# Optimization experiments

Measured on AMD Instinct MI355X. Metric: run time of the kernel, lower is better.

## Reference

```python
import jax, jax.numpy as jnp
import numpy as np


def setup_inputs() -> dict:
    key = jax.random.key(0)
    ks = jax.random.split(key, 6)
    B, C, H, W = 8, 64, 256, 256  # C*C == 4096 required by conv_du
    x = jax.random.normal(ks[0], (B, C, H, W), dtype=jnp.float32)
    W1 = jax.random.normal(ks[1], (16, 4096), dtype=jnp.float32) * 0.02  # Conv2d(4096,16,1) weight
    b1 = jax.random.normal(ks[2], (16,), dtype=jnp.float32) * 0.02
    W2 = jax.random.normal(ks[3], (4096, 16), dtype=jnp.float32) * 0.02  # Conv2d(16,4096,1) weight
    b2 = jax.random.normal(ks[4], (4096,), dtype=jnp.float32) * 0.02
    gamma = jax.random.normal(ks[5], (1,), dtype=jnp.float32) * 0.1  # nn.Parameter (init zeros in torch)
    return {"x": x, "W1": W1, "b1": b1, "W2": W2, "b2": b2, "gamma": gamma}


def reference(x, W1, b1, W2, b2, gamma):
    B, C, H, W = x.shape
    xf = x.reshape(B, C, H * W)  # (B, C, N)
    # Gram matrix over channels: energy[b,c,d] = <x_c, x_d>
    energy = jnp.einsum('bcn,bdn->bcd', xf, xf)
    # Diagonal cosine normalization (diag entries are sums of squares, >= 0)
    diag = jnp.sqrt(jnp.diagonal(energy, axis1=1, axis2=2))  # (B, C)
    energy = energy / diag[:, :, None] / diag[:, None, :]
    # SE-style 1x1 conv bottleneck on flattened C*C = 4096 channels
    h = jax.nn.relu(jnp.einsum('bk,ok->bo', energy.reshape(B, C * C), W1) + b1)
    energy = (jnp.einsum('bk,ok->bo', h, W2) + b2).reshape(B, C, C)
    # max-minus trick then softmax over last dim
    energy_new = jnp.max(energy, axis=-1, keepdims=True) - energy
    attention = jax.nn.softmax(energy_new, axis=-1)  # (B, C, C)
    out = jnp.einsum('bcd,bdn->bcn', attention, xf).reshape(B, C, H, W)
    return gamma * out + x
```

## Files before the change

kernel.cpp:

```cpp
#include <hip/hip_runtime.h>
#include <hip/hip_bf16.h>

#define CCH 64
#define NPIX 65536
#define NSPLIT 128
#define NB (NPIX / NSPLIT)

typedef short bf16x8 __attribute__((ext_vector_type(8)));
typedef float f32x16 __attribute__((ext_vector_type(16)));

static __device__ inline short f2bf(float f) {
    union { __hip_bfloat16 h; short s; } u;
    u.h = __float2bfloat16(f);
    return u.s;
}

static __device__ inline bf16x8 cvt8(float4 a, float4 b) {
    bf16x8 r;
    r[0] = f2bf(a.x); r[1] = f2bf(a.y); r[2] = f2bf(a.z); r[3] = f2bf(a.w);
    r[4] = f2bf(b.x); r[5] = f2bf(b.y); r[6] = f2bf(b.z); r[7] = f2bf(b.w);
    return r;
}

__global__ __launch_bounds__(256) void gram_kernel(const float* __restrict__ x,
                                                   float* __restrict__ gram) {
    const int b    = blockIdx.y;
    const int t    = threadIdx.x;
    const int wave = t >> 6, lane = t & 63;
    const int qi = wave >> 1, qj = wave & 1;
    const int lrow = lane & 31, khalf = lane >> 5;

    const float* xb = x + (size_t)b * CCH * NPIX;
    const int n0 = blockIdx.x * NB;
    const float* pa = xb + (size_t)(32 * qi + lrow) * NPIX + n0 + khalf * 8;
    const float* pb = xb + (size_t)(32 * qj + lrow) * NPIX + n0 + khalf * 8;

    f32x16 acc = {};
    #pragma unroll 4
    for (int k = 0; k < NB; k += 16) {
        float4 a0 = *(const float4*)(pa + k);
        float4 a1 = *(const float4*)(pa + k + 4);
        float4 b0 = *(const float4*)(pb + k);
        float4 b1 = *(const float4*)(pb + k + 4);
        acc = __builtin_amdgcn_mfma_f32_32x32x16_bf16(cvt8(a0, a1), cvt8(b0, b1), acc, 0, 0, 0);
    }

    float* g = gram + b * 4096;
    #pragma unroll
    for (int r = 0; r < 16; ++r) {
        int row = 32 * qi + 4 * khalf + (r & 3) + 8 * (r >> 2);
        atomicAdd(&g[row * 64 + 32 * qj + lrow], acc[r]);
    }
}

__global__ __launch_bounds__(256) void se_softmax_kernel(const float* __restrict__ gram,
                                                         const float* __restrict__ W1,
                                                         const float* __restrict__ b1,
                                                         const float* __restrict__ W2,
                                                         const float* __restrict__ b2,
                                                         float* __restrict__ attn) {
    __shared__ float e[4096];
    __shared__ float rs[64];
    __shared__ float hbuf[16];
    __shared__ float pw[4][16];
    __shared__ float rowred[64];
    const int b = blockIdx.x;
    const int t = threadIdx.x;
    const int wave = t >> 6, lane = t & 63;
    const float* g = gram + b * 4096;

    if (t < 64) rs[t] = rsqrtf(g[t * 65]);
    __syncthreads();

    #pragma unroll
    for (int j = 0; j < 4; ++j) {
        int l = j * 1024 + 4 * t;
        float4 gv = *(const float4*)(g + l);
        int c = l >> 6, d = l & 63;
        float rc = rs[c];
        float4 ev;
        ev.x = gv.x * rc * rs[d + 0];
        ev.y = gv.y * rc * rs[d + 1];
        ev.z = gv.z * rc * rs[d + 2];
        ev.w = gv.w * rc * rs[d + 3];
        *(float4*)(e + l) = ev;
    }
    __syncthreads();

    float acc[16] = {};
    #pragma unroll
    for (int j = 0; j < 4; ++j) {
        float4 ev = *(const float4*)(e + j * 1024 + 4 * t);
        #pragma unroll
        for (int o = 0; o < 16; ++o) {
            float4 wv = *(const float4*)(W1 + o * 4096 + j * 1024 + 4 * t);
            acc[o] += wv.x * ev.x + wv.y * ev.y + wv.z * ev.z + wv.w * ev.w;
        }
    }
    #pragma unroll
    for (int o = 0; o < 16; ++o) {
        #pragma unroll
        for (int off = 1; off < 64; off <<= 1)
            acc[o] += __shfl_xor(acc[o], off);
    }
    if (lane == 0) {
        #pragma unroll
        for (int o = 0; o < 16; ++o) pw[wave][o] = acc[o];
    }
    __syncthreads();
    if (t < 16) {
        float s = b1[t] + pw[0][t] + pw[1][t] + pw[2][t] + pw[3][t];
        hbuf[t] = fmaxf(s, 0.f);
    }
    __syncthreads();

    float hv[16];
    #pragma unroll
    for (int o = 0; o < 16; ++o) hv[o] = hbuf[o];
    for (int l = t; l < 4096; l += 256) {
        const float* w = W2 + (size_t)l * 16;
        float4 w0 = *(const float4*)(w);
        float4 w1v = *(const float4*)(w + 4);
        float4 w2v = *(const float4*)(w + 8);
        float4 w3v = *(const float4*)(w + 12);
        float s = b2[l]
            + w0.x * hv[0]  + w0.y * hv[1]  + w0.z * hv[2]  + w0.w * hv[3]
            + w1v.x * hv[4] + w1v.y * hv[5] + w1v.z * hv[6] + w1v.w * hv[7]
            + w2v.x * hv[8] + w2v.y * hv[9] + w2v.z * hv[10] + w2v.w * hv[11]
            + w3v.x * hv[12] + w3v.y * hv[13] + w3v.z * hv[14] + w3v.w * hv[15];
        e[l] = s;
    }
    __syncthreads();

    {
        int r = t >> 2, q = t & 3;
        float mn = INFINITY;
        #pragma unroll
        for (int j = 0; j < 16; ++j) mn = fminf(mn, e[r * 64 + q * 16 + j]);
        mn = fminf(mn, __shfl_xor(mn, 1));
        mn = fminf(mn, __shfl_xor(mn, 2));
        if (q == 0) rowred[r] = mn;
    }
    __syncthreads();
    for (int l = t; l < 4096; l += 256) {
        int c = l >> 6;
        e[l] = expf(rowred[c] - e[l]);
    }
    __syncthreads();
    {
        int r = t >> 2, q = t & 3;
        float s = 0.f;
        #pragma unroll
        for (int j = 0; j < 16; ++j) s += e[r * 64 + q * 16 + j];
        s += __shfl_xor(s, 1);
        s += __shfl_xor(s, 2);
        if (q == 0) rowred[r] = 1.0f / s;
    }
    __syncthreads();
    float* ab = attn + b * 4096;
    for (int l = t; l < 4096; l += 256) {
        int c = l >> 6;
        ab[l] = e[l] * rowred[c];
    }
}

__global__ __launch_bounds__(256) void apply_kernel(const float* __restrict__ x,
                                                    const float* __restrict__ attn,
                                                    const float* __restrict__ gamma,
                                                    float* __restrict__ out) {
    const int b    = blockIdx.y;
    const int t    = threadIdx.x;
    const int wave = t >> 6, lane = t & 63;
    const int ci = wave >> 1, nj = wave & 1;
    const int lrow = lane & 31, khalf = lane >> 5;
    const float gm = gamma[0];
    const float* xb = x + (size_t)b * CCH * NPIX;
    float* ob = out + (size_t)b * CCH * NPIX;

    const float* arow = attn + b * 4096 + (32 * ci + lrow) * 64 + khalf * 8;
    bf16x8 afrag[4];
    #pragma unroll
    for (int ks = 0; ks < 4; ++ks) {
        float4 a0 = *(const float4*)(arow + ks * 16);
        float4 a1 = *(const float4*)(arow + ks * 16 + 4);
        afrag[ks] = cvt8(a0, a1);
    }

    const int n0 = blockIdx.x * NB;
    for (int it = 0; it < NB / 64; ++it) {
        const int nc = n0 + it * 64 + nj * 32 + lrow;
        f32x16 acc = {};
        #pragma unroll
        for (int ks = 0; ks < 4; ++ks) {
            const int r0 = ks * 16 + khalf * 8;
            bf16x8 bfrag;
            #pragma unroll
            for (int i = 0; i < 8; ++i)
                bfrag[i] = f2bf(xb[(size_t)(r0 + i) * NPIX + nc]);
            acc = __builtin_amdgcn_mfma_f32_32x32x16_bf16(afrag[ks], bfrag, acc, 0, 0, 0);
        }
        #pragma unroll
        for (int r = 0; r < 16; ++r) {
            int c = 32 * ci + 4 * khalf + (r & 3) + 8 * (r >> 2);
            size_t off = (size_t)c * NPIX + nc;
            ob[off] = gm * acc[r] + xb[off];
        }
    }
}

extern "C" void kernel_launch(void* const* d_in, const int* in_sizes, int n_in,
                              void* d_out, int out_size, void* d_ws, size_t ws_size,
                              hipStream_t stream) {
    const float* x     = (const float*)d_in[0];
    const float* W1    = (const float*)d_in[1];
    const float* b1    = (const float*)d_in[2];
    const float* W2    = (const float*)d_in[3];
    const float* b2    = (const float*)d_in[4];
    const float* gamma = (const float*)d_in[5];
    float* out = (float*)d_out;

    float* gram = (float*)d_ws;
    float* attn = gram + 8 * 4096;

    hipMemsetAsync(d_ws, 0, 8 * 4096 * sizeof(float), stream);

    gram_kernel<<<dim3(NSPLIT, 8), 256, 0, stream>>>(x, gram);
    se_softmax_kernel<<<8, 256, 0, stream>>>(gram, W1, b1, W2, b2, attn);
    apply_kernel<<<dim3(NSPLIT, 8), 256, 0, stream>>>(x, attn, gamma, out);
}
```

Measured before the change: 306.0 us.

## Stage gram tiles in shared memory and retune apply kernel grid

The gram kernel now loads each 64x64 pixel tile of x once into padded LDS with coalesced float4 loads and feeds the MFMAs from there. Previously each wave fetched its own A and B rows straight from global memory, so every element was read several times with strided per-lane access. The apply kernel gets twice as many blocks along the pixel axis, and both kernels gain occupancy hints in their launch bounds. The cost is two block barriers per tile and some LDS usage.

After: 409.0 us. 33.7% more time.

```diff
diff --git a/kernel.cpp b/kernel.cpp
--- a/kernel.cpp
+++ b/kernel.cpp
@@ -3,8 +3,11 @@
 
 #define CCH 64
 #define NPIX 65536
-#define NSPLIT 128
-#define NB (NPIX / NSPLIT)
+#define NSPLIT_G 128
+#define NB_G (NPIX / NSPLIT_G)
+#define NSPLIT_A 256
+#define NB_A (NPIX / NSPLIT_A)
+#define NPAD 68
 
 typedef short bf16x8 __attribute__((ext_vector_type(8)));
 typedef float f32x16 __attribute__((ext_vector_type(16)));
@@ -22,8 +25,9 @@
     return r;
 }
 
-__global__ __launch_bounds__(256) void gram_kernel(const float* __restrict__ x,
-                                                   float* __restrict__ gram) {
+__global__ __launch_bounds__(256, 4) void gram_kernel(const float* __restrict__ x,
+                                                      float* __restrict__ gram) {
+    __shared__ float xs[64][NPAD];
     const int b    = blockIdx.y;
     const int t    = threadIdx.x;
     const int wave = t >> 6, lane = t & 63;
@@ -31,18 +35,30 @@
     const int lrow = lane & 31, khalf = lane >> 5;
 
     const float* xb = x + (size_t)b * CCH * NPIX;
-    const int n0 = blockIdx.x * NB;
-    const float* pa = xb + (size_t)(32 * qi + lrow) * NPIX + n0 + khalf * 8;
-    const float* pb = xb + (size_t)(32 * qj + lrow) * NPIX + n0 + khalf * 8;
+    const int n0 = blockIdx.x * NB_G;
+    const int sc = t >> 4, sq = 4 * (t & 15);
 
     f32x16 acc = {};
-    #pragma unroll 4
-    for (int k = 0; k < NB; k += 16) {
-        float4 a0 = *(const float4*)(pa + k);
-        float4 a1 = *(const float4*)(pa + k + 4);
-        float4 b0 = *(const float4*)(pb + k);
-        float4 b1 = *(const float4*)(pb + k + 4);
-        acc = __builtin_amdgcn_mfma_f32_32x32x16_bf16(cvt8(a0, a1), cvt8(b0, b1), acc, 0, 0, 0);
+    for (int tile = 0; tile < NB_G / 64; ++tile) {
+        const int nt = n0 + tile * 64;
+        float4 v[4];
+        #pragma unroll
+        for (int i = 0; i < 4; ++i)
+            v[i] = *(const float4*)(xb + (size_t)(sc + 16 * i) * NPIX + nt + sq);
+        __syncthreads();
+        #pragma unroll
+        for (int i = 0; i < 4; ++i)
+            *(float4*)(&xs[sc + 16 * i][sq]) = v[i];
+        __syncthreads();
+
+        #pragma unroll
+        for (int kk = 0; kk < 64; kk += 16) {
+            const float* pa = &xs[32 * qi + lrow][kk + 8 * khalf];
+            const float* pb = &xs[32 * qj + lrow][kk + 8 * khalf];
+            float4 a0 = *(const float4*)(pa), a1 = *(const float4*)(pa + 4);
+            float4 b0 = *(const float4*)(pb), b1 = *(const float4*)(pb + 4);
+            acc = __builtin_amdgcn_mfma_f32_32x32x16_bf16(cvt8(a0, a1), cvt8(b0, b1), acc, 0, 0, 0);
+        }
     }
 
     float* g = gram + b * 4096;
@@ -164,10 +180,10 @@
     }
 }
 
-__global__ __launch_bounds__(256) void apply_kernel(const float* __restrict__ x,
-                                                    const float* __restrict__ attn,
-                                                    const float* __restrict__ gamma,
-                                                    float* __restrict__ out) {
+__global__ __launch_bounds__(256, 8) void apply_kernel(const float* __restrict__ x,
+                                                       const float* __restrict__ attn,
+                                                       const float* __restrict__ gamma,
+                                                       float* __restrict__ out) {
     const int b    = blockIdx.y;
     const int t    = threadIdx.x;
     const int wave = t >> 6, lane = t & 63;
@@ -186,8 +202,8 @@
         afrag[ks] = cvt8(a0, a1);
     }
 
-    const int n0 = blockIdx.x * NB;
-    for (int it = 0; it < NB / 64; ++it) {
+    const int n0 = blockIdx.x * NB_A;
+    for (int it = 0; it < NB_A / 64; ++it) {
         const int nc = n0 + it * 64 + nj * 32 + lrow;
         f32x16 acc = {};
         #pragma unroll
@@ -224,7 +240,7 @@
 
     hipMemsetAsync(d_ws, 0, 8 * 4096 * sizeof(float), stream);
 
-    gram_kernel<<<dim3(NSPLIT, 8), 256, 0, stream>>>(x, gram);
+    gram_kernel<<<dim3(NSPLIT_G, 8), 256, 0, stream>>>(x, gram);
     se_softmax_kernel<<<8, 256, 0, stream>>>(gram, W1, b1, W2, b2, attn);
-    apply_kernel<<<dim3(NSPLIT, 8), 256, 0, stream>>>(x, attn, gamma, out);
-}
+    apply_kernel<<<dim3(NSPLIT_A, 8), 256, 0, stream>>>(x, attn, gamma, out);
+}
```
